# Performance work log

Hardware: AMD Instinct MI355X
Metric: run time of the kernel (lower is better)

The kernel has to match this reference:

```python
import jax, jax.numpy as jnp
import numpy as np
import math

SEQ, BATCH, HID, HEADS = 2048, 2, 2048, 16
HEAD_DIM = HID // HEADS
ROPE_BASE = 10000.0


def setup_inputs() -> dict:
    key = jax.random.key(0)
    k1, k2, k3 = jax.random.split(key, 3)
    hidden_states = jax.random.normal(k1, (SEQ, BATCH, HID), dtype=jnp.float32)
    # causal mask: True means masked (gpt2-style attention_mask_func fills with -10000)
    attention_mask = jnp.triu(jnp.ones((SEQ, SEQ), dtype=bool), k=1)[None, None, :, :]
    w_qkv = jax.random.normal(k2, (3 * HID, HID), dtype=jnp.float32) * 0.02
    b_qkv = jnp.zeros((3 * HID,), dtype=jnp.float32)
    w_dense = jax.random.normal(k3, (HID, HID), dtype=jnp.float32) * 0.02
    b_dense = jnp.zeros((HID,), dtype=jnp.float32)
    return {"hidden_states": hidden_states, "attention_mask": attention_mask,
            "w_qkv": w_qkv, "b_qkv": b_qkv, "w_dense": w_dense, "b_dense": b_dense}


def _rotary_cos_sin(seq_len, dim, dtype):
    inv_freq = 1.0 / (ROPE_BASE ** (jnp.arange(0, dim, 2, dtype=jnp.float32) / dim))
    t = jnp.arange(seq_len, dtype=jnp.float32)
    freqs = jnp.einsum("s,d->sd", t, inv_freq)
    emb = jnp.concatenate([freqs, freqs], axis=-1)  # [s, dim]
    # broadcast to [s, 1, 1, dim] over (batch, heads)
    return jnp.cos(emb)[:, None, None, :].astype(dtype), jnp.sin(emb)[:, None, None, :].astype(dtype)


def _rotate_half(x):
    x1, x2 = jnp.split(x, 2, axis=-1)
    return jnp.concatenate([-x2, x1], axis=-1)


def reference(hidden_states, attention_mask, w_qkv, b_qkv, w_dense, b_dense):
    s, b, h = hidden_states.shape
    # QKV projection: [s, b, 3h] -> [s, b, nh, 3*hd] -> split
    mixed = hidden_states @ w_qkv.T + b_qkv
    mixed = mixed.reshape(s, b, HEADS, 3 * HEAD_DIM)
    q, k, v = jnp.split(mixed, 3, axis=-1)  # each [s, b, nh, hd]
    # rotary (rotary_pct == 1 -> full head dim)
    cos, sin = _rotary_cos_sin(s, HEAD_DIM, q.dtype)
    q = q * cos + _rotate_half(q) * sin
    k = k * cos + _rotate_half(k) * sin
    # attention scores [b, nh, s_q, s_k]
    norm_factor = math.sqrt(HEAD_DIM)
    scores = jnp.einsum("sbhd,tbhd->bhst", q, k) / norm_factor
    scores = jnp.where(attention_mask, jnp.asarray(-10000.0, scores.dtype), scores)
    # softmax in fp32
    probs = jax.nn.softmax(scores.astype(jnp.float32), axis=-1).astype(scores.dtype)
    # context [s, b, nh, hd] -> [s, b, h]
    context = jnp.einsum("bhst,tbhd->sbhd", probs, v).reshape(s, b, h)
    # dense with skip_bias_add: bias returned separately
    output = context @ w_dense.T
    return output, b_dense
```

## Files before the change

### kernel.cpp

```cpp
#include <hip/hip_runtime.h>
#include <cstdint>
#include <math.h>


typedef unsigned short u16;
typedef __bf16 bf16x8 __attribute__((ext_vector_type(8)));
typedef float floatx4 __attribute__((ext_vector_type(4)));

#define SEQ 2048
#define BATCH 2
#define HID 2048
#define NH 16
#define HD 128
#define LDA 72
#define LDK 136

__device__ __forceinline__ u16 f2bf(float f) {
  union { float f; uint32_t u; } v; v.f = f;
  uint32_t u = v.u;
  return (u16)((u + 0x7FFFu + ((u >> 16) & 1u)) >> 16);
}

__device__ __forceinline__ void st8_bf16(u16* dst, const float* s) {
  uint32_t pk[4];
#pragma unroll
  for (int j = 0; j < 4; j++)
    pk[j] = (uint32_t)f2bf(s[2 * j]) | ((uint32_t)f2bf(s[2 * j + 1]) << 16);
  *(uint4*)dst = make_uint4(pk[0], pk[1], pk[2], pk[3]);
}

__device__ __forceinline__ void gl16(const u16* g, u16* l) {
  __builtin_amdgcn_global_load_lds(
      (const __attribute__((address_space(1))) void*)g,
      (__attribute__((address_space(3))) void*)l, 16, 0, 0);
}

__global__ __launch_bounds__(256) void cvt_inputs(
    const float* __restrict__ W, const float* __restrict__ Hid,
    u16* __restrict__ wb, u16* __restrict__ Ah) {
  const int blk = blockIdx.x;
  const int c0 = threadIdx.x * 8;
  const float* src;
  u16* dst;
  if (blk < 4096) {
    int dt = blk >> 7, r = blk & 127;
    int srow = (dt < 16) ? ((dt * 3 + 1) * 128 + r) : (((dt - 16) * 3) * 128 + r);
    src = W + (size_t)srow * HID;
    dst = wb + (size_t)blk * HID;
  } else {
    int r = blk - 4096;
    src = Hid + (size_t)r * HID;
    dst = Ah + (size_t)r * HID;
  }
  float t[8];
  *(floatx4*)&t[0] = *(const floatx4*)(src + c0);
  *(floatx4*)&t[4] = *(const floatx4*)(src + c0 + 4);
  st8_bf16(dst + c0, t);
}

__global__ __launch_bounds__(256) void cvt_wd(const float* __restrict__ W,
                                              u16* __restrict__ wd) {
  const int r = blockIdx.x;
  const int c0 = threadIdx.x * 8;
  float t[8];
  const float* src = W + (size_t)r * HID;
  *(floatx4*)&t[0] = *(const floatx4*)(src + c0);
  *(floatx4*)&t[4] = *(const floatx4*)(src + c0 + 4);
  st8_bf16(wd + (size_t)r * HID + c0, t);
}

__global__ __launch_bounds__(256, 2) void qkv_qk(
    const u16* __restrict__ Ah, const u16* __restrict__ wb,
    const float* __restrict__ bias, u16* __restrict__ Qw,
    u16* __restrict__ Kw) {
  __shared__ __align__(16) u16 As[128 * 64];
  __shared__ __align__(16) u16 Bs[128 * 64];
  const int tid = threadIdx.x;
  const int wv = tid >> 6, lane = tid & 63;
  const int quad = lane >> 4, l16 = lane & 15;
  const int wt = blockIdx.x;
  const int bm = blockIdx.y;
  const int rowA0 = bm * 128;
  const int wm = (wv >> 1) * 64;
  const int wn = (wv & 1) * 32;
  const int ntoff[4] = {wn, wn + 16, wn + 64, wn + 80};

  const int lrow = wv * 32 + (lane >> 3);
  const int lcol = (lane & 7) * 8;
  const u16* Ag = Ah + (size_t)(rowA0 + lrow) * HID + lcol;
  const u16* Bg = wb + ((size_t)wt * 128 + lrow) * HID + lcol;
  u16* Al = &As[(wv * 32) * 64];
  u16* Bl = &Bs[(wv * 32) * 64];

  floatx4 acc[4][4];
#pragma unroll
  for (int i = 0; i < 4; i++)
#pragma unroll
    for (int j = 0; j < 4; j++) acc[i][j] = (floatx4){0.f, 0.f, 0.f, 0.f};

  for (int kb = 0; kb < HID; kb += 64) {
#pragma unroll
    for (int j = 0; j < 4; j++) {
      gl16(Ag + (size_t)j * 8 * HID + kb, Al + j * 8 * 64);
      gl16(Bg + (size_t)j * 8 * HID + kb, Bl + j * 8 * 64);
    }
    __syncthreads();
#pragma unroll
    for (int ks = 0; ks < 64; ks += 32) {
      bf16x8 af[4], bfr[4];
#pragma unroll
      for (int mi = 0; mi < 4; mi++)
        af[mi] = *(const bf16x8*)&As[(wm + mi * 16 + l16) * 64 + ks + quad * 8];
#pragma unroll
      for (int ni = 0; ni < 4; ni++)
        bfr[ni] = *(const bf16x8*)&Bs[(ntoff[ni] + l16) * 64 + ks + quad * 8];
#pragma unroll
      for (int mi = 0; mi < 4; mi++)
#pragma unroll
        for (int ni = 0; ni < 4; ni++)
          acc[mi][ni] = __builtin_amdgcn_mfma_f32_16x16x32_bf16(
              af[mi], bfr[ni], acc[mi][ni], 0, 0, 0);
    }
    __syncthreads();
  }

  const int seg = (wt < 16) ? 1 : 0;
  const int head = wt & 15;
  u16* dst = seg ? Kw : Qw;
  float bv[4];
#pragma unroll
  for (int ni = 0; ni < 4; ni++)
    bv[ni] = bias[(head * 3 + seg) * 128 + ntoff[ni] + l16];
  const float RC = 0.20762050593045951f;
  const float f0 = exp2f(-(float)(wn + l16) * RC);
  const float f1 = exp2f(-(float)(wn + 16 + l16) * RC);

#pragma unroll
  for (int mi = 0; mi < 4; mi++) {
#pragma unroll
    for (int reg = 0; reg < 4; reg++) {
      int r = rowA0 + wm + mi * 16 + quad * 4 + reg;
      int s = r >> 1, b = r & 1;
      size_t base = ((size_t)(b * NH + head) * SEQ + s) * HD;
      float sv, cv;
      sincosf((float)s * f0, &sv, &cv);
      {
        float lo = acc[mi][0][reg] + bv[0];
        float hi = acc[mi][2][reg] + bv[2];
        dst[base + wn + l16] = f2bf(lo * cv - hi * sv);
        dst[base + wn + l16 + 64] = f2bf(hi * cv + lo * sv);
      }
      sincosf((float)s * f1, &sv, &cv);
      {
        float lo = acc[mi][1][reg] + bv[1];
        float hi = acc[mi][3][reg] + bv[3];
        dst[base + wn + 16 + l16] = f2bf(lo * cv - hi * sv);
        dst[base + wn + 16 + l16 + 64] = f2bf(hi * cv + lo * sv);
      }
    }
  }
}

__global__ __launch_bounds__(256, 2) void qkv_v(
    const u16* __restrict__ Ah, const float* __restrict__ W,
    const float* __restrict__ bias, u16* __restrict__ Vt) {
  __shared__ __align__(16) u16 As[128 * 64];
  __shared__ __align__(16) u16 Bs[128 * LDA];
  const int tid = threadIdx.x;
  const int wv = tid >> 6, lane = tid & 63;
  const int quad = lane >> 4, l16 = lane & 15;
  const int head = blockIdx.x;
  const int bm = blockIdx.y;
  const int rowA0 = bm * 128;
  const int rowB0 = (head * 3 + 2) * 128;
  const int wm = (wv >> 1) * 64;
  const int wn = (wv & 1) * 32;
  const int ntoff[4] = {wn, wn + 16, wn + 64, wn + 80};

  const int lrow = wv * 32 + (lane >> 3);
  const int lcol = (lane & 7) * 8;
  const u16* Ag = Ah + (size_t)(rowA0 + lrow) * HID + lcol;
  u16* Al = &As[(wv * 32) * 64];

  floatx4 acc[4][4];
#pragma unroll
  for (int i = 0; i < 4; i++)
#pragma unroll
    for (int j = 0; j < 4; j++) acc[i][j] = (floatx4){0.f, 0.f, 0.f, 0.f};

  for (int kb = 0; kb < HID; kb += 64) {
    float fb[4][8];
#pragma unroll
    for (int i = 0; i < 4; i++) {
      int c = i * 256 + tid;
      int row = c >> 3, k8 = (c & 7) * 8;
      const float* sb = &W[(size_t)(rowB0 + row) * HID + kb + k8];
      *(floatx4*)&fb[i][0] = *(const floatx4*)sb;
      *(floatx4*)&fb[i][4] = *(const floatx4*)(sb + 4);
    }
    __syncthreads();
#pragma unroll
    for (int j = 0; j < 4; j++)
      gl16(Ag + (size_t)j * 8 * HID + kb, Al + j * 8 * 64);
#pragma unroll
    for (int i = 0; i < 4; i++) {
      int c = i * 256 + tid;
      int row = c >> 3, k8 = (c & 7) * 8;
      st8_bf16(&Bs[row * LDA + k8], fb[i]);
    }
    __syncthreads();
#pragma unroll
    for (int ks = 0; ks < 64; ks += 32) {
      bf16x8 af[4], bfr[4];
#pragma unroll
      for (int mi = 0; mi < 4; mi++)
        af[mi] = *(const bf16x8*)&As[(wm + mi * 16 + l16) * 64 + ks + quad * 8];
#pragma unroll
      for (int ni = 0; ni < 4; ni++)
        bfr[ni] = *(const bf16x8*)&Bs[(ntoff[ni] + l16) * LDA + ks + quad * 8];
#pragma unroll
      for (int mi = 0; mi < 4; mi++)
#pragma unroll
        for (int ni = 0; ni < 4; ni++)
          acc[mi][ni] = __builtin_amdgcn_mfma_f32_16x16x32_bf16(
              af[mi], bfr[ni], acc[mi][ni], 0, 0, 0);
    }
  }
  __syncthreads();

  float bv[4];
#pragma unroll
  for (int ni = 0; ni < 4; ni++)
    bv[ni] = bias[(head * 3 + 2) * 128 + ntoff[ni] + l16];
#pragma unroll
  for (int mi = 0; mi < 4; mi++) {
#pragma unroll
    for (int ni = 0; ni < 4; ni++) {
      int d = ntoff[ni] + l16;
#pragma unroll
      for (int reg = 0; reg < 4; reg++) {
        int r = rowA0 + wm + mi * 16 + quad * 4 + reg;
        int s = r >> 1, b = r & 1;
        Vt[((size_t)(b * NH + head) * HD + d) * SEQ + s] =
            f2bf(acc[mi][ni][reg] + bv[ni]);
      }
    }
  }
}

__global__ __launch_bounds__(256, 2) void attn(
    const u16* __restrict__ Qw, const u16* __restrict__ Kw,
    const u16* __restrict__ Vt, u16* __restrict__ ctx) {
  __shared__ __align__(16) u16 Ks[64 * LDK];
  __shared__ __align__(16) u16 Vs[128 * LDA];
  __shared__ __align__(16) u16 Pl[4 * 32 * 72];

  const int tid = threadIdx.x;
  const int wv = tid >> 6, lane = tid & 63;
  const int quad = lane >> 4, l16 = lane & 15;
  const int bh = blockIdx.y;
  const int b = bh >> 4, h = bh & 15;
  const int qt = (gridDim.x - 1) - blockIdx.x;
  const int sw = qt * 128 + wv * 32;
  const size_t bhoff = (size_t)bh * SEQ * HD;

  bf16x8 qf[2][4];
#pragma unroll
  for (int mi = 0; mi < 2; mi++)
#pragma unroll
    for (int kc = 0; kc < 4; kc++)
      qf[mi][kc] = *(const bf16x8*)&Qw[bhoff +
                                       (size_t)(sw + mi * 16 + l16) * HD +
                                       kc * 32 + quad * 8];

  floatx4 o[2][8];
#pragma unroll
  for (int mi = 0; mi < 2; mi++)
#pragma unroll
    for (int ni = 0; ni < 8; ni++) o[mi][ni] = (floatx4){0.f, 0.f, 0.f, 0.f};
  float mst[2][4], lst[2][4];
#pragma unroll
  for (int mi = 0; mi < 2; mi++)
#pragma unroll
    for (int r = 0; r < 4; r++) { mst[mi][r] = -1e30f; lst[mi][r] = 0.f; }

  const int nt = qt * 2 + 2;
  const float inv_norm = 0.088388347648318447f;

  for (int t = 0; t < nt; t++) {
    bf16x8 tk[4], tv[4];
#pragma unroll
    for (int i = 0; i < 4; i++) {
      int c = i * 256 + tid;
      tk[i] = *(const bf16x8*)&Kw[bhoff + (size_t)(t * 64 + (c >> 4)) * HD +
                                  (c & 15) * 8];
      tv[i] = *(const bf16x8*)&Vt[bhoff + (size_t)(c >> 3) * SEQ + t * 64 +
                                  (c & 7) * 8];
    }
    __syncthreads();
#pragma unroll
    for (int i = 0; i < 4; i++) {
      int c = i * 256 + tid;
      *(bf16x8*)&Ks[(c >> 4) * LDK + (c & 15) * 8] = tk[i];
      *(bf16x8*)&Vs[(c >> 3) * LDA + (c & 7) * 8] = tv[i];
    }
    __syncthreads();

    const bool active = (t * 64 <= sw + 31);
    if (active) {
      floatx4 sa[2][4];
#pragma unroll
      for (int mi = 0; mi < 2; mi++)
#pragma unroll
        for (int ni = 0; ni < 4; ni++) sa[mi][ni] = (floatx4){0.f, 0.f, 0.f, 0.f};
#pragma unroll
      for (int kc = 0; kc < 4; kc++) {
        bf16x8 kf[4];
#pragma unroll
        for (int ni = 0; ni < 4; ni++)
          kf[ni] = *(const bf16x8*)&Ks[(ni * 16 + l16) * LDK + kc * 32 + quad * 8];
#pragma unroll
        for (int mi = 0; mi < 2; mi++)
#pragma unroll
          for (int ni = 0; ni < 4; ni++)
            sa[mi][ni] = __builtin_amdgcn_mfma_f32_16x16x32_bf16(
                qf[mi][kc], kf[ni], sa[mi][ni], 0, 0, 0);
      }
      float alpha[2][4];
#pragma unroll
      for (int mi = 0; mi < 2; mi++) {
#pragma unroll
        for (int reg = 0; reg < 4; reg++) {
          int sq = sw + mi * 16 + quad * 4 + reg;
          float rv[4];
#pragma unroll
          for (int ni = 0; ni < 4; ni++) {
            int sk = t * 64 + ni * 16 + l16;
            float v = sa[mi][ni][reg] * inv_norm;
            if (sk > sq) v = -10000.0f;
            rv[ni] = v;
          }
          float rmax = fmaxf(fmaxf(rv[0], rv[1]), fmaxf(rv[2], rv[3]));
          rmax = fmaxf(rmax, __shfl_xor(rmax, 1));
          rmax = fmaxf(rmax, __shfl_xor(rmax, 2));
          rmax = fmaxf(rmax, __shfl_xor(rmax, 4));
          rmax = fmaxf(rmax, __shfl_xor(rmax, 8));
          float mn = fmaxf(mst[mi][reg], rmax);
          float al = expf(mst[mi][reg] - mn);
          float rs = 0.f;
#pragma unroll
          for (int ni = 0; ni < 4; ni++) {
            float p = expf(rv[ni] - mn);
            rs += p;
            Pl[wv * 2304 + (mi * 16 + quad * 4 + reg) * 72 + ni * 16 + l16] =
                f2bf(p);
          }
          rs += __shfl_xor(rs, 1);
          rs += __shfl_xor(rs, 2);
          rs += __shfl_xor(rs, 4);
          rs += __shfl_xor(rs, 8);
          lst[mi][reg] = lst[mi][reg] * al + rs;
          mst[mi][reg] = mn;
          alpha[mi][reg] = al;
        }
      }
#pragma unroll
      for (int mi = 0; mi < 2; mi++)
#pragma unroll
        for (int ni = 0; ni < 8; ni++)
#pragma unroll
          for (int reg = 0; reg < 4; reg++)
            o[mi][ni][reg] *= alpha[mi][reg];
    }
    __syncthreads();
    if (active) {
#pragma unroll
      for (int kc = 0; kc < 2; kc++) {
        bf16x8 pf[2];
#pragma unroll
        for (int mi = 0; mi < 2; mi++)
          pf[mi] = *(const bf16x8*)&Pl[wv * 2304 + (mi * 16 + l16) * 72 +
                                       kc * 32 + quad * 8];
#pragma unroll
        for (int ni = 0; ni < 8; ni++) {
          bf16x8 vf =
              *(const bf16x8*)&Vs[(ni * 16 + l16) * LDA + kc * 32 + quad * 8];
#pragma unroll
          for (int mi = 0; mi < 2; mi++)
            o[mi][ni] = __builtin_amdgcn_mfma_f32_16x16x32_bf16(
                pf[mi], vf, o[mi][ni], 0, 0, 0);
        }
      }
    }
  }

#pragma unroll
  for (int mi = 0; mi < 2; mi++) {
#pragma unroll
    for (int reg = 0; reg < 4; reg++) {
      float inv = 1.0f / lst[mi][reg];
      int sq = sw + mi * 16 + quad * 4 + reg;
      size_t rbase = ((size_t)(sq * BATCH + b)) * HID + h * HD;
#pragma unroll
      for (int ni = 0; ni < 8; ni++)
        ctx[rbase + ni * 16 + l16] = f2bf(o[mi][ni][reg] * inv);
    }
  }
}

__global__ __launch_bounds__(256, 2) void dense_gemm(
    const u16* __restrict__ A, const u16* __restrict__ Wd,
    float* __restrict__ out) {
  __shared__ __align__(16) u16 As[128 * 64];
  __shared__ __align__(16) u16 Bs[128 * 64];
  const int tid = threadIdx.x;
  const int wv = tid >> 6, lane = tid & 63;
  const int quad = lane >> 4, l16 = lane & 15;
  const int bn = blockIdx.x, bm = blockIdx.y;
  const int rowA0 = bm * 128, rowB0 = bn * 128;
  const int wm = (wv >> 1) * 64;
  const int wn = (wv & 1) * 64;
  const int ntoff[4] = {wn, wn + 16, wn + 32, wn + 48};

  const int lrow = wv * 32 + (lane >> 3);
  const int lcol = (lane & 7) * 8;
  const u16* Ag = A + (size_t)(rowA0 + lrow) * HID + lcol;
  const u16* Bg = Wd + (size_t)(rowB0 + lrow) * HID + lcol;
  u16* Al = &As[(wv * 32) * 64];
  u16* Bl = &Bs[(wv * 32) * 64];

  floatx4 acc[4][4];
#pragma unroll
  for (int i = 0; i < 4; i++)
#pragma unroll
    for (int j = 0; j < 4; j++) acc[i][j] = (floatx4){0.f, 0.f, 0.f, 0.f};

  for (int kb = 0; kb < HID; kb += 64) {
#pragma unroll
    for (int j = 0; j < 4; j++) {
      gl16(Ag + (size_t)j * 8 * HID + kb, Al + j * 8 * 64);
      gl16(Bg + (size_t)j * 8 * HID + kb, Bl + j * 8 * 64);
    }
    __syncthreads();
#pragma unroll
    for (int ks = 0; ks < 64; ks += 32) {
      bf16x8 af[4], bfr[4];
#pragma unroll
      for (int mi = 0; mi < 4; mi++)
        af[mi] = *(const bf16x8*)&As[(wm + mi * 16 + l16) * 64 + ks + quad * 8];
#pragma unroll
      for (int ni = 0; ni < 4; ni++)
        bfr[ni] = *(const bf16x8*)&Bs[(ntoff[ni] + l16) * 64 + ks + quad * 8];
#pragma unroll
      for (int mi = 0; mi < 4; mi++)
#pragma unroll
        for (int ni = 0; ni < 4; ni++)
          acc[mi][ni] = __builtin_amdgcn_mfma_f32_16x16x32_bf16(
              af[mi], bfr[ni], acc[mi][ni], 0, 0, 0);
    }
    __syncthreads();
  }

#pragma unroll
  for (int mi = 0; mi < 4; mi++)
#pragma unroll
    for (int reg = 0; reg < 4; reg++) {
      int r = rowA0 + wm + mi * 16 + quad * 4 + reg;
#pragma unroll
      for (int ni = 0; ni < 4; ni++)
        out[(size_t)r * HID + bn * 128 + ntoff[ni] + l16] = acc[mi][ni][reg];
    }
}

__global__ void copy_bias(const float* __restrict__ bd, float* __restrict__ out) {
  int i = blockIdx.x * 256 + threadIdx.x;
  if (i < HID) out[(size_t)SEQ * BATCH * HID + i] = bd[i];
}

extern "C" void kernel_launch(void* const* d_in, const int* in_sizes, int n_in,
                              void* d_out, int out_size, void* d_ws,
                              size_t ws_size, hipStream_t stream) {
  const float *hidden = nullptr, *w_qkv = nullptr, *b_qkv = nullptr;
  const float *w_dense = nullptr, *b_dense = nullptr;
  for (int i = 0; i < n_in; i++) {
    long s = in_sizes[i];
    if (s == 8388608L) hidden = (const float*)d_in[i];
    else if (s == 12582912L) w_qkv = (const float*)d_in[i];
    else if (s == 6144L) b_qkv = (const float*)d_in[i];
    else if (s == 4194304L) w_dense = (const float*)d_in[i];
    else if (s == 2048L) b_dense = (const float*)d_in[i];
  }
  float* out = (float*)d_out;

  char* ws = (char*)d_ws;
  u16* Qw = (u16*)(ws);
  u16* Kw = (u16*)(ws + 16777216ll);
  u16* Vt = (u16*)(ws + 33554432ll);
  u16* wb = (u16*)(ws + 33554432ll);
  u16* Ah = (u16*)(ws + 50331648ll);
  u16* ctx = (u16*)(ws + 50331648ll);
  u16* wd = (u16*)(ws);

  cvt_inputs<<<dim3(8192), dim3(256), 0, stream>>>(w_qkv, hidden, wb, Ah);
  qkv_qk<<<dim3(32, 32), dim3(256), 0, stream>>>(Ah, wb, b_qkv, Qw, Kw);
  qkv_v<<<dim3(16, 32), dim3(256), 0, stream>>>(Ah, w_qkv, b_qkv, Vt);
  attn<<<dim3(16, 32), dim3(256), 0, stream>>>(Qw, Kw, Vt, ctx);
  cvt_wd<<<dim3(2048), dim3(256), 0, stream>>>(w_dense, wd);
  dense_gemm<<<dim3(16, 32), dim3(256), 0, stream>>>(ctx, wd, out);
  copy_bias<<<dim3(8), dim3(256), 0, stream>>>(b_dense, out);
}
```

Baseline: 514.3 us.

## Restructure attention kernel: 8 waves, register-prefetched K/V, exp2 softmax, swizzled P

Measured after the change: 551.3 us. +7.2%, slower.

```diff
diff --git a/kernel.cpp b/kernel.cpp
--- a/kernel.cpp
+++ b/kernel.cpp
@@ -248,163 +248,178 @@
   }
 }
 
-__global__ __launch_bounds__(256, 2) void attn(
+__global__ __launch_bounds__(512, 4) void attn(
     const u16* __restrict__ Qw, const u16* __restrict__ Kw,
     const u16* __restrict__ Vt, u16* __restrict__ ctx) {
   __shared__ __align__(16) u16 Ks[64 * LDK];
   __shared__ __align__(16) u16 Vs[128 * LDA];
-  __shared__ __align__(16) u16 Pl[4 * 32 * 72];
+  __shared__ __align__(16) u16 Pl[8 * 16 * 64];
 
   const int tid = threadIdx.x;
   const int wv = tid >> 6, lane = tid & 63;
   const int quad = lane >> 4, l16 = lane & 15;
-  const int bh = blockIdx.y;
+
+  const int L = blockIdx.x;
+  int bh, qt;
+  if (L < 256) { bh = L >> 3; qt = 15 - (L & 7); }
+  else         { bh = (L - 256) >> 3; qt = (L - 256) & 7; }
   const int b = bh >> 4, h = bh & 15;
-  const int qt = (gridDim.x - 1) - blockIdx.x;
-  const int sw = qt * 128 + wv * 32;
+  const int sw = qt * 128 + wv * 16;
   const size_t bhoff = (size_t)bh * SEQ * HD;
-
-  bf16x8 qf[2][4];
-#pragma unroll
-  for (int mi = 0; mi < 2; mi++)
-#pragma unroll
-    for (int kc = 0; kc < 4; kc++)
-      qf[mi][kc] = *(const bf16x8*)&Qw[bhoff +
-                                       (size_t)(sw + mi * 16 + l16) * HD +
-                                       kc * 32 + quad * 8];
-
-  floatx4 o[2][8];
-#pragma unroll
-  for (int mi = 0; mi < 2; mi++)
-#pragma unroll
-    for (int ni = 0; ni < 8; ni++) o[mi][ni] = (floatx4){0.f, 0.f, 0.f, 0.f};
-  float mst[2][4], lst[2][4];
-#pragma unroll
-  for (int mi = 0; mi < 2; mi++)
-#pragma unroll
-    for (int r = 0; r < 4; r++) { mst[mi][r] = -1e30f; lst[mi][r] = 0.f; }
+  const int pw = wv * 1024;
+
+  bf16x8 qf[4];
+#pragma unroll
+  for (int kc = 0; kc < 4; kc++)
+    qf[kc] = *(const bf16x8*)&Qw[bhoff + (size_t)(sw + l16) * HD + kc * 32 +
+                                 quad * 8];
+
+  floatx4 o[8];
+#pragma unroll
+  for (int ni = 0; ni < 8; ni++) o[ni] = (floatx4){0.f, 0.f, 0.f, 0.f};
+  float mst[4], lst[4];
+#pragma unroll
+  for (int r = 0; r < 4; r++) { mst[r] = -1e30f; lst[r] = 0.f; }
 
   const int nt = qt * 2 + 2;
-  const float inv_norm = 0.088388347648318447f;
+  const float SCL2 = 0.088388347648318447f * 1.442695040888963f;
+  const float MSK2 = -10000.0f * 1.442695040888963f;
+
+  bf16x8 tkA[2], tvA[2], tkB[2], tvB[2];
+#pragma unroll
+  for (int i = 0; i < 2; i++) {
+    int c = i * 512 + tid;
+    tkA[i] = *(const bf16x8*)&Kw[bhoff + (size_t)(c >> 4) * HD + (c & 15) * 8];
+    tvA[i] = *(const bf16x8*)&Vt[bhoff + (size_t)(c >> 3) * SEQ + (c & 7) * 8];
+  }
 
   for (int t = 0; t < nt; t++) {
-    bf16x8 tk[4], tv[4];
-#pragma unroll
-    for (int i = 0; i < 4; i++) {
-      int c = i * 256 + tid;
-      tk[i] = *(const bf16x8*)&Kw[bhoff + (size_t)(t * 64 + (c >> 4)) * HD +
-                                  (c & 15) * 8];
-      tv[i] = *(const bf16x8*)&Vt[bhoff + (size_t)(c >> 3) * SEQ + t * 64 +
-                                  (c & 7) * 8];
-    }
-    __syncthreads();
-#pragma unroll
-    for (int i = 0; i < 4; i++) {
-      int c = i * 256 + tid;
-      *(bf16x8*)&Ks[(c >> 4) * LDK + (c & 15) * 8] = tk[i];
-      *(bf16x8*)&Vs[(c >> 3) * LDA + (c & 7) * 8] = tv[i];
-    }
-    __syncthreads();
-
-    const bool active = (t * 64 <= sw + 31);
+    __syncthreads();
+    if (t & 1) {
+#pragma unroll
+      for (int i = 0; i < 2; i++) {
+        int c = i * 512 + tid;
+        *(bf16x8*)&Ks[(c >> 4) * LDK + (c & 15) * 8] = tkB[i];
+        *(bf16x8*)&Vs[(c >> 3) * LDA + (c & 7) * 8] = tvB[i];
+      }
+      if (t + 1 < nt) {
+#pragma unroll
+        for (int i = 0; i < 2; i++) {
+          int c = i * 512 + tid;
+          tkA[i] = *(const bf16x8*)&Kw[bhoff +
+                                       (size_t)((t + 1) * 64 + (c >> 4)) * HD +
+                                       (c & 15) * 8];
+          tvA[i] = *(const bf16x8*)&Vt[bhoff + (size_t)(c >> 3) * SEQ +
+                                       (t + 1) * 64 + (c & 7) * 8];
+        }
+      }
+    } else {
+#pragma unroll
+      for (int i = 0; i < 2; i++) {
+        int c = i * 512 + tid;
+        *(bf16x8*)&Ks[(c >> 4) * LDK + (c & 15) * 8] = tkA[i];
+        *(bf16x8*)&Vs[(c >> 3) * LDA + (c & 7) * 8] = tvA[i];
+      }
+      if (t + 1 < nt) {
+#pragma unroll
+        for (int i = 0; i < 2; i++) {
+          int c = i * 512 + tid;
+          tkB[i] = *(const bf16x8*)&Kw[bhoff +
+                                       (size_t)((t + 1) * 64 + (c >> 4)) * HD +
+                                       (c & 15) * 8];
+          tvB[i] = *(const bf16x8*)&Vt[bhoff + (size_t)(c >> 3) * SEQ +
+                                       (t + 1) * 64 + (c & 7) * 8];
+        }
+      }
+    }
+    __syncthreads();
+
+    const bool active = (t * 64 <= sw + 15);
     if (active) {
-      floatx4 sa[2][4];
-#pragma unroll
-      for (int mi = 0; mi < 2; mi++)
-#pragma unroll
-        for (int ni = 0; ni < 4; ni++) sa[mi][ni] = (floatx4){0.f, 0.f, 0.f, 0.f};
+      floatx4 sa[4];
+#pragma unroll
+      for (int ni = 0; ni < 4; ni++) sa[ni] = (floatx4){0.f, 0.f, 0.f, 0.f};
+      __builtin_amdgcn_s_setprio(1);
 #pragma unroll
       for (int kc = 0; kc < 4; kc++) {
         bf16x8 kf[4];
 #pragma unroll
         for (int ni = 0; ni < 4; ni++)
-          kf[ni] = *(const bf16x8*)&Ks[(ni * 16 + l16) * LDK + kc * 32 + quad * 8];
-#pragma unroll
-        for (int mi = 0; mi < 2; mi++)
-#pragma unroll
-          for (int ni = 0; ni < 4; ni++)
-            sa[mi][ni] = __builtin_amdgcn_mfma_f32_16x16x32_bf16(
-                qf[mi][kc], kf[ni], sa[mi][ni], 0, 0, 0);
-      }
-      float alpha[2][4];
-#pragma unroll
-      for (int mi = 0; mi < 2; mi++) {
-#pragma unroll
-        for (int reg = 0; reg < 4; reg++) {
-          int sq = sw + mi * 16 + quad * 4 + reg;
-          float rv[4];
-#pragma unroll
-          for (int ni = 0; ni < 4; ni++) {
-            int sk = t * 64 + ni * 16 + l16;
-            float v = sa[mi][ni][reg] * inv_norm;
-            if (sk > sq) v = -10000.0f;
-            rv[ni] = v;
-          }
-          float rmax = fmaxf(fmaxf(rv[0], rv[1]), fmaxf(rv[2], rv[3]));
-          rmax = fmaxf(rmax, __shfl_xor(rmax, 1));
-          rmax = fmaxf(rmax, __shfl_xor(rmax, 2));
-          rmax = fmaxf(rmax, __shfl_xor(rmax, 4));
-          rmax = fmaxf(rmax, __shfl_xor(rmax, 8));
-          float mn = fmaxf(mst[mi][reg], rmax);
-          float al = expf(mst[mi][reg] - mn);
-          float rs = 0.f;
-#pragma unroll
-          for (int ni = 0; ni < 4; ni++) {
-            float p = expf(rv[ni] - mn);
-            rs += p;
-            Pl[wv * 2304 + (mi * 16 + quad * 4 + reg) * 72 + ni * 16 + l16] =
-                f2bf(p);
-          }
-          rs += __shfl_xor(rs, 1);
-          rs += __shfl_xor(rs, 2);
-          rs += __shfl_xor(rs, 4);
-          rs += __shfl_xor(rs, 8);
-          lst[mi][reg] = lst[mi][reg] * al + rs;
-          mst[mi][reg] = mn;
-          alpha[mi][reg] = al;
+          kf[ni] =
+              *(const bf16x8*)&Ks[(ni * 16 + l16) * LDK + kc * 32 + quad * 8];
+#pragma unroll
+        for (int ni = 0; ni < 4; ni++)
+          sa[ni] = __builtin_amdgcn_mfma_f32_16x16x32_bf16(qf[kc], kf[ni],
+                                                           sa[ni], 0, 0, 0);
+      }
+      __builtin_amdgcn_s_setprio(0);
+
+      float alpha[4];
+#pragma unroll
+      for (int reg = 0; reg < 4; reg++) {
+        int sq = sw + quad * 4 + reg;
+        int rr = quad * 4 + reg;
+        float rv[4];
+#pragma unroll
+        for (int ni = 0; ni < 4; ni++) {
+          int sk = t * 64 + ni * 16 + l16;
+          float v = sa[ni][reg] * SCL2;
+          if (sk > sq) v = MSK2;
+          rv[ni] = v;
         }
-      }
-#pragma unroll
-      for (int mi = 0; mi < 2; mi++)
-#pragma unroll
-        for (int ni = 0; ni < 8; ni++)
-#pragma unroll
-          for (int reg = 0; reg < 4; reg++)
-            o[mi][ni][reg] *= alpha[mi][reg];
-    }
-    __syncthreads();
-    if (active) {
+        float rmax = fmaxf(fmaxf(rv[0], rv[1]), fmaxf(rv[2], rv[3]));
+        rmax = fmaxf(rmax, __shfl_xor(rmax, 1));
+        rmax = fmaxf(rmax, __shfl_xor(rmax, 2));
+        rmax = fmaxf(rmax, __shfl_xor(rmax, 4));
+        rmax = fmaxf(rmax, __shfl_xor(rmax, 8));
+        float mn = fmaxf(mst[reg], rmax);
+        float al = exp2f(mst[reg] - mn);
+        float rs = 0.f;
+#pragma unroll
+        for (int ni = 0; ni < 4; ni++) {
+          float p = exp2f(rv[ni] - mn);
+          rs += p;
+          Pl[pw + rr * 64 + (((ni * 16 + l16)) ^ ((rr & 7) << 3))] = f2bf(p);
+        }
+        rs += __shfl_xor(rs, 1);
+        rs += __shfl_xor(rs, 2);
+        rs += __shfl_xor(rs, 4);
+        rs += __shfl_xor(rs, 8);
+        lst[reg] = lst[reg] * al + rs;
+        mst[reg] = mn;
+        alpha[reg] = al;
+      }
+#pragma unroll
+      for (int ni = 0; ni < 8; ni++)
+#pragma unroll
+        for (int reg = 0; reg < 4; reg++) o[ni][reg] *= alpha[reg];
+
+      __builtin_amdgcn_s_setprio(1);
 #pragma unroll
       for (int kc = 0; kc < 2; kc++) {
-        bf16x8 pf[2];
-#pragma unroll
-        for (int mi = 0; mi < 2; mi++)
-          pf[mi] = *(const bf16x8*)&Pl[wv * 2304 + (mi * 16 + l16) * 72 +
-                                       kc * 32 + quad * 8];
+        bf16x8 pf = *(const bf16x8*)&Pl[pw + l16 * 64 +
+                                        ((kc * 32 + quad * 8) ^
+                                         ((l16 & 7) << 3))];
 #pragma unroll
         for (int ni = 0; ni < 8; ni++) {
           bf16x8 vf =
               *(const bf16x8*)&Vs[(ni * 16 + l16) * LDA + kc * 32 + quad * 8];
-#pragma unroll
-          for (int mi = 0; mi < 2; mi++)
-            o[mi][ni] = __builtin_amdgcn_mfma_f32_16x16x32_bf16(
-                pf[mi], vf, o[mi][ni], 0, 0, 0);
+          o[ni] = __builtin_amdgcn_mfma_f32_16x16x32_bf16(pf, vf, o[ni], 0, 0,
+                                                          0);
         }
       }
-    }
-  }
-
-#pragma unroll
-  for (int mi = 0; mi < 2; mi++) {
-#pragma unroll
-    for (int reg = 0; reg < 4; reg++) {
-      float inv = 1.0f / lst[mi][reg];
-      int sq = sw + mi * 16 + quad * 4 + reg;
-      size_t rbase = ((size_t)(sq * BATCH + b)) * HID + h * HD;
-#pragma unroll
-      for (int ni = 0; ni < 8; ni++)
-        ctx[rbase + ni * 16 + l16] = f2bf(o[mi][ni][reg] * inv);
-    }
+      __builtin_amdgcn_s_setprio(0);
+    }
+  }
+
+#pragma unroll
+  for (int reg = 0; reg < 4; reg++) {
+    float inv = 1.0f / lst[reg];
+    int sq = sw + quad * 4 + reg;
+    size_t rbase = ((size_t)(sq * BATCH + b)) * HID + h * HD;
+#pragma unroll
+    for (int ni = 0; ni < 8; ni++)
+      ctx[rbase + ni * 16 + l16] = f2bf(o[ni][reg] * inv);
   }
 }
 
@@ -504,7 +519,7 @@
   cvt_inputs<<<dim3(8192), dim3(256), 0, stream>>>(w_qkv, hidden, wb, Ah);
   qkv_qk<<<dim3(32, 32), dim3(256), 0, stream>>>(Ah, wb, b_qkv, Qw, Kw);
   qkv_v<<<dim3(16, 32), dim3(256), 0, stream>>>(Ah, w_qkv, b_qkv, Vt);
-  attn<<<dim3(16, 32), dim3(256), 0, stream>>>(Qw, Kw, Vt, ctx);
+  attn<<<dim3(512), dim3(512), 0, stream>>>(Qw, Kw, Vt, ctx);
   cvt_wd<<<dim3(2048), dim3(256), 0, stream>>>(w_dense, wd);
   dense_gemm<<<dim3(16, 32), dim3(256), 0, stream>>>(ctx, wd, out);
   copy_bias<<<dim3(8), dim3(256), 0, stream>>>(b_dense, out);
```

## Use direct global-to-LDS loads with XOR swizzle, exp2 softmax, and priority hints in attention

Applied to the files above, without the earlier changes.

Measured after the change: 460.0 us. -10.6%, faster.

```diff
diff --git a/kernel.cpp b/kernel.cpp
--- a/kernel.cpp
+++ b/kernel.cpp
@@ -13,7 +13,6 @@
 #define NH 16
 #define HD 128
 #define LDA 72
-#define LDK 136
 
 __device__ __forceinline__ u16 f2bf(float f) {
   union { float f; uint32_t u; } v; v.f = f;
@@ -251,8 +250,8 @@
 __global__ __launch_bounds__(256, 2) void attn(
     const u16* __restrict__ Qw, const u16* __restrict__ Kw,
     const u16* __restrict__ Vt, u16* __restrict__ ctx) {
-  __shared__ __align__(16) u16 Ks[64 * LDK];
-  __shared__ __align__(16) u16 Vs[128 * LDA];
+  __shared__ __align__(16) u16 Ks[64 * 128];
+  __shared__ __align__(16) u16 Vs[128 * 64];
   __shared__ __align__(16) u16 Pl[4 * 32 * 72];
 
   const int tid = threadIdx.x;
@@ -260,7 +259,7 @@
   const int quad = lane >> 4, l16 = lane & 15;
   const int bh = blockIdx.y;
   const int b = bh >> 4, h = bh & 15;
-  const int qt = (gridDim.x - 1) - blockIdx.x;
+  const int qt = (bh < 16) ? blockIdx.x : 15 - blockIdx.x;
   const int sw = qt * 128 + wv * 32;
   const size_t bhoff = (size_t)bh * SEQ * HD;
 
@@ -285,24 +284,20 @@
     for (int r = 0; r < 4; r++) { mst[mi][r] = -1e30f; lst[mi][r] = 0.f; }
 
   const int nt = qt * 2 + 2;
-  const float inv_norm = 0.088388347648318447f;
+  const float SCL2 = 0.088388347648318447f * 1.442695040888963f;
+  const float MSK2 = -10000.0f * 1.442695040888963f;
 
   for (int t = 0; t < nt; t++) {
-    bf16x8 tk[4], tv[4];
+    __syncthreads();
 #pragma unroll
     for (int i = 0; i < 4; i++) {
       int c = i * 256 + tid;
-      tk[i] = *(const bf16x8*)&Kw[bhoff + (size_t)(t * 64 + (c >> 4)) * HD +
-                                  (c & 15) * 8];
-      tv[i] = *(const bf16x8*)&Vt[bhoff + (size_t)(c >> 3) * SEQ + t * 64 +
-                                  (c & 7) * 8];
-    }
-    __syncthreads();
-#pragma unroll
-    for (int i = 0; i < 4; i++) {
-      int c = i * 256 + tid;
-      *(bf16x8*)&Ks[(c >> 4) * LDK + (c & 15) * 8] = tk[i];
-      *(bf16x8*)&Vs[(c >> 3) * LDA + (c & 7) * 8] = tv[i];
+      int rk = c >> 4, uk = c & 15;
+      gl16(&Kw[bhoff + (size_t)(t * 64 + rk) * HD + (uk ^ (rk & 7)) * 8],
+           &Ks[(i * 256 + wv * 64) * 8]);
+      int rv = c >> 3, uv = c & 7;
+      gl16(&Vt[bhoff + (size_t)rv * SEQ + t * 64 + (uv ^ (rv & 7)) * 8],
+           &Vs[(i * 256 + wv * 64) * 8]);
     }
     __syncthreads();
 
@@ -313,12 +308,14 @@
       for (int mi = 0; mi < 2; mi++)
 #pragma unroll
         for (int ni = 0; ni < 4; ni++) sa[mi][ni] = (floatx4){0.f, 0.f, 0.f, 0.f};
+      __builtin_amdgcn_s_setprio(1);
 #pragma unroll
       for (int kc = 0; kc < 4; kc++) {
         bf16x8 kf[4];
 #pragma unroll
         for (int ni = 0; ni < 4; ni++)
-          kf[ni] = *(const bf16x8*)&Ks[(ni * 16 + l16) * LDK + kc * 32 + quad * 8];
+          kf[ni] = *(const bf16x8*)&Ks[(ni * 16 + l16) * 128 +
+                                       (((kc * 4 + quad) ^ (l16 & 7)) * 8)];
 #pragma unroll
         for (int mi = 0; mi < 2; mi++)
 #pragma unroll
@@ -326,6 +323,8 @@
             sa[mi][ni] = __builtin_amdgcn_mfma_f32_16x16x32_bf16(
                 qf[mi][kc], kf[ni], sa[mi][ni], 0, 0, 0);
       }
+      __builtin_amdgcn_s_setprio(0);
+
       float alpha[2][4];
 #pragma unroll
       for (int mi = 0; mi < 2; mi++) {
@@ -336,8 +335,8 @@
 #pragma unroll
           for (int ni = 0; ni < 4; ni++) {
             int sk = t * 64 + ni * 16 + l16;
-            float v = sa[mi][ni][reg] * inv_norm;
-            if (sk > sq) v = -10000.0f;
+            float v = sa[mi][ni][reg] * SCL2;
+            if (sk > sq) v = MSK2;
             rv[ni] = v;
           }
           float rmax = fmaxf(fmaxf(rv[0], rv[1]), fmaxf(rv[2], rv[3]));
@@ -346,11 +345,11 @@
           rmax = fmaxf(rmax, __shfl_xor(rmax, 4));
           rmax = fmaxf(rmax, __shfl_xor(rmax, 8));
           float mn = fmaxf(mst[mi][reg], rmax);
-          float al = expf(mst[mi][reg] - mn);
+          float al = exp2f(mst[mi][reg] - mn);
           float rs = 0.f;
 #pragma unroll
           for (int ni = 0; ni < 4; ni++) {
-            float p = expf(rv[ni] - mn);
+            float p = exp2f(rv[ni] - mn);
             rs += p;
             Pl[wv * 2304 + (mi * 16 + quad * 4 + reg) * 72 + ni * 16 + l16] =
                 f2bf(p);
@@ -371,9 +370,8 @@
 #pragma unroll
           for (int reg = 0; reg < 4; reg++)
             o[mi][ni][reg] *= alpha[mi][reg];
-    }
-    __syncthreads();
-    if (active) {
+
+      __builtin_amdgcn_s_setprio(1);
 #pragma unroll
       for (int kc = 0; kc < 2; kc++) {
         bf16x8 pf[2];
@@ -383,14 +381,15 @@
                                        kc * 32 + quad * 8];
 #pragma unroll
         for (int ni = 0; ni < 8; ni++) {
-          bf16x8 vf =
-              *(const bf16x8*)&Vs[(ni * 16 + l16) * LDA + kc * 32 + quad * 8];
+          bf16x8 vf = *(const bf16x8*)&Vs[(ni * 16 + l16) * 64 +
+                                          (((kc * 4 + quad) ^ (l16 & 7)) * 8)];
 #pragma unroll
           for (int mi = 0; mi < 2; mi++)
             o[mi][ni] = __builtin_amdgcn_mfma_f32_16x16x32_bf16(
                 pf[mi], vf, o[mi][ni], 0, 0, 0);
         }
       }
+      __builtin_amdgcn_s_setprio(0);
     }
   }
 
```
